# Kernel tuning notes

Measured on AMD Instinct MI355X. Metric: run time of the kernel, lower is better.

The kernel has to match this reference:

```python
import jax, jax.numpy as jnp
import numpy as np

N_NODES, N_EDGES, BATCH, F_IN, GENES = 65536, 262144, 2048, 78, 735
HEADS, HID = 8, 64            # gnn_out_dim = HEADS*HID = 512
GOUT = HEADS * HID
NEG_SLOPE = 0.2
BN_EPS = 1e-5


def setup_inputs() -> dict:
    key = jax.random.key(0)
    ks = jax.random.split(key, 24)
    sc = lambda k, shp, fan: (jax.random.normal(k, shp, jnp.float32) / np.sqrt(fan)).astype(jnp.float32)
    d = {}
    d["x"] = jax.random.normal(ks[0], (N_NODES, F_IN), jnp.float32)
    d["edge_index"] = jax.random.randint(ks[1], (2, N_EDGES), 0, N_NODES)
    d["batch"] = jnp.sort(jax.random.randint(ks[2], (N_NODES,), 0, BATCH))
    d["x_gen"] = jax.random.normal(ks[3], (BATCH, GENES), jnp.float32)
    # GATConv 1: in=78 -> heads*hid
    d["W1"] = sc(ks[4], (F_IN, GOUT), F_IN)
    d["att_src1"] = sc(ks[5], (HEADS, HID), HID)
    d["att_dst1"] = sc(ks[6], (HEADS, HID), HID)
    d["bias1"] = jnp.zeros((GOUT,), jnp.float32)
    # GATConv 2: in=512 -> heads*hid
    d["W2"] = sc(ks[7], (GOUT, GOUT), GOUT)
    d["att_src2"] = sc(ks[8], (HEADS, HID), HID)
    d["att_dst2"] = sc(ks[9], (HEADS, HID), HID)
    d["bias2"] = jnp.zeros((GOUT,), jnp.float32)
    # geno encoder: Linear(735,128) -> BN -> ReLU -> Linear(128,512) -> ReLU
    d["gW1"] = sc(ks[10], (GENES, 2 * HID), GENES)
    d["gb1"] = jnp.zeros((2 * HID,), jnp.float32)
    d["bn_gamma"] = jnp.ones((2 * HID,), jnp.float32)
    d["bn_beta"] = jnp.zeros((2 * HID,), jnp.float32)
    d["bn_mean"] = jnp.zeros((2 * HID,), jnp.float32)
    d["bn_var"] = jnp.ones((2 * HID,), jnp.float32)
    d["gW2"] = sc(ks[11], (2 * HID, GOUT), 2 * HID)
    d["gb2"] = jnp.zeros((GOUT,), jnp.float32)
    # fusion MLP: 1024 -> 256 -> 128 -> 1
    d["fW1"] = sc(ks[12], (2 * GOUT, 256), 2 * GOUT)
    d["fb1"] = jnp.zeros((256,), jnp.float32)
    d["fW2"] = sc(ks[13], (256, 128), 256)
    d["fb2"] = jnp.zeros((128,), jnp.float32)
    d["fW3"] = sc(ks[14], (128, 1), 128)
    d["fb3"] = jnp.zeros((1,), jnp.float32)
    return d


def gat_layer(x, edge_index, W, att_src, att_dst, bias):
    """PyG GATConv (concat=True, add_self_loops=True), eval mode (no dropout)."""
    N = x.shape[0]
    H, C = att_src.shape
    h = (x @ W).reshape(N, H, C)                      # [N,H,C]
    a_src = jnp.einsum('nhc,hc->nh', h, att_src)      # [N,H]
    a_dst = jnp.einsum('nhc,hc->nh', h, att_dst)      # [N,H]
    loop = jnp.arange(N)
    src = jnp.concatenate([edge_index[0], loop])      # [E+N]
    dst = jnp.concatenate([edge_index[1], loop])
    e = jax.nn.leaky_relu(a_src[src] + a_dst[dst], NEG_SLOPE)   # [E+N,H]
    # scatter-softmax over incoming edges per destination node
    e_max = jax.ops.segment_max(e, dst, num_segments=N)
    e = jnp.exp(e - e_max[dst])
    denom = jax.ops.segment_sum(e, dst, num_segments=N)
    alpha = e / (denom[dst] + 1e-16)                  # [E+N,H]
    msg = h[src] * alpha[:, :, None]                  # [E+N,H,C]
    out = jax.ops.segment_sum(msg, dst, num_segments=N)  # [N,H,C]
    return out.reshape(N, H * C) + bias


def global_mean_pool(x, batch, num_graphs):
    sums = jax.ops.segment_sum(x, batch, num_segments=num_graphs)
    cnt = jax.ops.segment_sum(jnp.ones((x.shape[0],), x.dtype), batch, num_segments=num_graphs)
    return sums / jnp.maximum(cnt, 1.0)[:, None]


def reference(x, edge_index, batch, x_gen,
              W1, att_src1, att_dst1, bias1,
              W2, att_src2, att_dst2, bias2,
              gW1, gb1, bn_gamma, bn_beta, bn_mean, bn_var, gW2, gb2,
              fW1, fb1, fW2, fb2, fW3, fb3):
    h = jax.nn.elu(gat_layer(x, edge_index, W1, att_src1, att_dst1, bias1))
    h = jax.nn.elu(gat_layer(h, edge_index, W2, att_src2, att_dst2, bias2))
    g = global_mean_pool(h, batch, BATCH)             # [B, 512]
    # genomic encoder (eval-mode BatchNorm with running stats)
    z = x_gen @ gW1 + gb1
    z = (z - bn_mean) * jax.lax.rsqrt(bn_var + BN_EPS) * bn_gamma + bn_beta
    z = jax.nn.relu(z)
    z = jax.nn.relu(z @ gW2 + gb2)                    # [B, 512]
    c = jnp.concatenate([g, z], axis=1)               # [B, 1024]
    c = jax.nn.relu(c @ fW1 + fb1)
    c = jax.nn.relu(c @ fW2 + fb2)
    return c @ fW3 + fb3                              # [B, 1]
```

## Files before the change

kernel.cpp:

```cpp
#include <hip/hip_runtime.h>
#include <hip/hip_bf16.h>
#include <cstdint>
#include <cstddef>

#define NN 65536
#define NE 262144
#define NB 2048
#define FIN 78
#define GOUTD 512

typedef __bf16 bf16x8 __attribute__((ext_vector_type(8)));
typedef float f32x4 __attribute__((ext_vector_type(4)));

__device__ __forceinline__ float leaky02(float x) { return x > 0.f ? x : 0.2f * x; }
__device__ __forceinline__ void atomAddF(float* p, float v) { unsafeAtomicAdd(p, v); }

__global__ void k_hist(const int* __restrict__ dst, int* __restrict__ deg) {
    int i = blockIdx.x * 256 + threadIdx.x;
    if (i < NE) atomicAdd(&deg[dst[i]], 1);
}

__global__ void k_scan_block(const int* __restrict__ deg, int* __restrict__ ex, int* __restrict__ bsum) {
    __shared__ int s[256];
    int t = threadIdx.x; int g = blockIdx.x * 256 + t;
    int v = deg[g];
    s[t] = v; __syncthreads();
    for (int d = 1; d < 256; d <<= 1) {
        int x = (t >= d) ? s[t - d] : 0;
        __syncthreads();
        s[t] += x;
        __syncthreads();
    }
    ex[g] = s[t] - v;
    if (t == 255) bsum[blockIdx.x] = s[t];
}

__global__ void k_scan_add2(int* __restrict__ rowptr, const int* __restrict__ bsum) {
    __shared__ int s[256];
    int t = threadIdx.x;
    int v = bsum[t];
    s[t] = v; __syncthreads();
    for (int d = 1; d < 256; d <<= 1) {
        int x = (t >= d) ? s[t - d] : 0;
        __syncthreads();
        s[t] += x;
        __syncthreads();
    }
    int prefix = (blockIdx.x == 0) ? 0 : s[blockIdx.x - 1];
    int i = blockIdx.x * 256 + t;
    rowptr[i] += prefix;
    if (i == 0) rowptr[NN] = NE;
}

__global__ void k_scatter(const int* __restrict__ src, const int* __restrict__ dst,
                          const int* __restrict__ rowptr, int* __restrict__ fill,
                          int* __restrict__ colI) {
    int i = blockIdx.x * 256 + threadIdx.x;
    if (i < NE) {
        int d = dst[i];
        int pos = rowptr[d] + atomicAdd(&fill[d], 1);
        colI[pos] = src[i];
    }
}

__global__ void k_cvt_prep(const float* __restrict__ x, const float* __restrict__ W1,
                           const float* __restrict__ W2, __hip_bfloat16* __restrict__ xb,
                           __hip_bfloat16* __restrict__ w1t, __hip_bfloat16* __restrict__ w2t,
                           int* __restrict__ deg, int* __restrict__ fill,
                           const int* __restrict__ batch, int* __restrict__ gstart)
{
    int blk = blockIdx.x;
    if (blk < 16384) {
        int i = blk * 256 + threadIdx.x;
        int row = i >> 6;
        int c = (i & 63) << 1;
        float v0 = (c < FIN) ? x[(size_t)row * FIN + c] : 0.f;
        float v1 = (c + 1 < FIN) ? x[(size_t)row * FIN + c + 1] : 0.f;
        __hip_bfloat16 o[2];
        o[0] = __float2bfloat16(v0);
        o[1] = __float2bfloat16(v1);
        *(uint32_t*)&xb[(size_t)row * 128 + c] = *(const uint32_t*)o;
    } else if (blk < 16640) {
        int i = (blk - 16384) * 256 + threadIdx.x;
        int n = i >> 7, k = i & 127;
        w1t[i] = __float2bfloat16(k < FIN ? W1[(size_t)k * 512 + n] : 0.f);
    } else if (blk < 17664) {
        int i = (blk - 16640) * 256 + threadIdx.x;
        int n = i >> 9, k = i & 511;
        w2t[i] = __float2bfloat16(W2[(size_t)k * 512 + n]);
    } else {
        int i = (blk - 17664) * 256 + threadIdx.x;
        if (i < NN) {
            deg[i] = 0; fill[i] = 0;
            int cur = batch[i];
            int prev = (i == 0) ? -1 : batch[i - 1];
            for (int g = prev + 1; g <= cur; ++g) gstart[g] = i;
            if (i == NN - 1) {
                for (int g = cur + 1; g <= NB; ++g) gstart[g] = NN;
            }
        }
    }
}

__global__ __launch_bounds__(256) void k_mfma_gemm(
    const __hip_bfloat16* __restrict__ A, const __hip_bfloat16* __restrict__ BT,
    __hip_bfloat16* __restrict__ C, int K,
    const float* __restrict__ att_src, const float* __restrict__ att_dst,
    float* __restrict__ a_src, float* __restrict__ a_dst,
    float* __restrict__ t1, float* __restrict__ t2,
    const float* __restrict__ fb1, const float* __restrict__ fb2,
    float* __restrict__ z1)
{
    __shared__ __hip_bfloat16 smem[128 * 128];
    __hip_bfloat16* As = smem;
    __hip_bfloat16* Bs = smem + 128 * 64;
    int tid = threadIdx.x;
    int lane = tid & 63;
    int wave = tid >> 6;
    int id = blockIdx.x;
    int m0 = (((id >> 5) << 3) + (id & 7)) * 128;
    int n0 = ((id >> 3) & 3) * 128;
    int wm = (wave >> 1) * 64;
    int wn = (wave & 1) * 64;
    f32x4 acc[4][4] = {};

    int swz = lane & 7;

    for (int k0 = 0; k0 < K; k0 += 64) {
        #pragma unroll
        for (int c = 0; c < 4; ++c) {
            int off = c * 4096 + tid * 16;
            int r = off >> 7;
            int c16 = (off >> 4) & 7;
            int c16s = c16 ^ (r & 7);
            __builtin_amdgcn_global_load_lds(
                (const __attribute__((address_space(1))) void*)(A + (size_t)(m0 + r) * K + k0 + c16s * 8),
                (__attribute__((address_space(3))) void*)((char*)As + off), 16, 0, 0);
            __builtin_amdgcn_global_load_lds(
                (const __attribute__((address_space(1))) void*)(BT + (size_t)(n0 + r) * K + k0 + c16s * 8),
                (__attribute__((address_space(3))) void*)((char*)Bs + off), 16, 0, 0);
        }
        __syncthreads();
        #pragma unroll
        for (int kk = 0; kk < 64; kk += 32) {
            int c16r = (kk >> 3) + (lane >> 4);
            bf16x8 af[4], bfr[4];
            #pragma unroll
            for (int t = 0; t < 4; ++t) {
                int ra = wm + t * 16 + (lane & 15);
                int rb = wn + t * 16 + (lane & 15);
                af[t]  = *(const bf16x8*)((char*)As + ra * 128 + ((c16r ^ swz) << 4));
                bfr[t] = *(const bf16x8*)((char*)Bs + rb * 128 + ((c16r ^ swz) << 4));
            }
            #pragma unroll
            for (int i = 0; i < 4; ++i)
                #pragma unroll
                for (int j = 0; j < 4; ++j)
                    acc[i][j] = __builtin_amdgcn_mfma_f32_16x16x32_bf16(af[i], bfr[j], acc[i][j], 0, 0, 0);
        }
        __syncthreads();
    }

    int rowb = wm + ((lane >> 4) << 2);
    int colb = wn + (lane & 15);
    #pragma unroll
    for (int i = 0; i < 4; ++i) {
        #pragma unroll
        for (int j = 0; j < 4; ++j) {
            int cc = colb + j * 16;
            #pragma unroll
            for (int r = 0; r < 4; ++r) {
                int rr = rowb + i * 16 + r;
                int word = (cc >> 1) ^ (((rr >> 2) & 7) << 3);
                smem[rr * 128 + word * 2 + (cc & 1)] = __float2bfloat16(acc[i][j][r]);
            }
        }
    }
    __syncthreads();
    #pragma unroll
    for (int cc2 = 0; cc2 < 8; ++cc2) {
        int p = cc2 * 256 + tid;
        int rr = p >> 4;
        int c16 = p & 15;
        int x = ((rr >> 2) & 7) << 3;
        bf16x8 v = *(const bf16x8*)((char*)smem + rr * 256 + ((((c16 << 2) ^ x)) << 2));
        *(bf16x8*)(C + (size_t)(m0 + rr) * 512 + n0 + c16 * 8) = v;
        const float* sp = att_src + n0 + c16 * 8;
        const float* dp = att_dst + n0 + c16 * 8;
        float4 s0 = *(const float4*)sp, s1 = *(const float4*)(sp + 4);
        float4 d0 = *(const float4*)dp, d1 = *(const float4*)(dp + 4);
        float sv[8] = {s0.x, s0.y, s0.z, s0.w, s1.x, s1.y, s1.z, s1.w};
        float dv[8] = {d0.x, d0.y, d0.z, d0.w, d1.x, d1.y, d1.z, d1.w};
        float ps = 0.f, pd = 0.f;
        #pragma unroll
        for (int k = 0; k < 8; ++k) {
            float f = (float)v[k];
            ps = fmaf(f, sv[k], ps);
            pd = fmaf(f, dv[k], pd);
        }
        #pragma unroll
        for (int d = 1; d < 8; d <<= 1) {
            ps += __shfl_xor(ps, d);
            pd += __shfl_xor(pd, d);
        }
        if ((c16 & 7) == 0) {
            int head = (n0 >> 6) + (c16 >> 3);
            a_src[(size_t)(m0 + rr) * 8 + head] = ps;
            a_dst[(size_t)(m0 + rr) * 8 + head] = pd;
        }
    }

    if (t1) {
        if (tid < 64)  *(float4*)(t1 + (size_t)id * 256 + tid * 4) = *(const float4*)(fb1 + tid * 4);
        if (tid < 32)  *(float4*)(t2 + (size_t)id * 128 + tid * 4) = *(const float4*)(fb2 + tid * 4);
        if (tid >= 64 && tid < 96)
            *(float4*)(z1 + (size_t)id * 128 + (tid - 64) * 4) = make_float4(0.f, 0.f, 0.f, 0.f);
    }
}

__global__ __launch_bounds__(256) void k_gat_agg(
    const __hip_bfloat16* __restrict__ h, const float* __restrict__ asrc,
    const float* __restrict__ adst, const int* __restrict__ rowptr,
    const int* __restrict__ colI, const float* __restrict__ bias,
    __hip_bfloat16* __restrict__ out)
{
    int lane = threadIdx.x & 63;
    int n = blockIdx.x * 4 + (threadIdx.x >> 6);
    int start = rowptr[n], end = rowptr[n + 1];
    int hh = lane >> 3;
    float adst_h = adst[n * 8 + hh];
    float acc[8];
    float wsum;
    {
        float w = __expf(leaky02(asrc[n * 8 + hh] + adst_h));
        wsum = w;
        bf16x8 v = *(const bf16x8*)(h + (size_t)n * GOUTD + lane * 8);
        #pragma unroll
        for (int j = 0; j < 8; ++j) acc[j] = w * (float)v[j];
    }
    int i = start;
    for (; i + 1 < end; i += 2) {
        int s0 = colI[i];
        int s1 = colI[i + 1];
        float w0 = __expf(leaky02(asrc[s0 * 8 + hh] + adst_h));
        float w1 = __expf(leaky02(asrc[s1 * 8 + hh] + adst_h));
        bf16x8 v0 = *(const bf16x8*)(h + (size_t)s0 * GOUTD + lane * 8);
        bf16x8 v1 = *(const bf16x8*)(h + (size_t)s1 * GOUTD + lane * 8);
        wsum += w0 + w1;
        #pragma unroll
        for (int j = 0; j < 8; ++j)
            acc[j] = fmaf(w0, (float)v0[j], fmaf(w1, (float)v1[j], acc[j]));
    }
    if (i < end) {
        int s = colI[i];
        float w = __expf(leaky02(asrc[s * 8 + hh] + adst_h));
        wsum += w;
        bf16x8 v = *(const bf16x8*)(h + (size_t)s * GOUTD + lane * 8);
        #pragma unroll
        for (int j = 0; j < 8; ++j) acc[j] = fmaf(w, (float)v[j], acc[j]);
    }
    float rden = 1.f / (wsum + 1e-16f);
    const float* bp = bias + lane * 8;
    float4 b0 = *(const float4*)bp, b1 = *(const float4*)(bp + 4);
    float bb[8] = {b0.x, b0.y, b0.z, b0.w, b1.x, b1.y, b1.z, b1.w};
    __hip_bfloat16 o[8] __attribute__((aligned(16)));
    #pragma unroll
    for (int j = 0; j < 8; ++j) {
        float v = fmaf(acc[j], rden, bb[j]);
        v = (v > 0.f) ? v : (__expf(v) - 1.f);
        o[j] = __float2bfloat16(v);
    }
    *(bf16x8*)(out + (size_t)n * GOUTD + lane * 8) = *(const bf16x8*)o;
}

__global__ __launch_bounds__(512) void k_gat_agg_pool(
    const __hip_bfloat16* __restrict__ h, const float* __restrict__ asrc,
    const float* __restrict__ adst, const int* __restrict__ rowptr,
    const int* __restrict__ colI, const float* __restrict__ bias,
    const int* __restrict__ gstart, float* __restrict__ cfeat)
{
    __shared__ float red[8][512];
    int lane = threadIdx.x & 63;
    int wv = threadIdx.x >> 6;
    int g = blockIdx.x;
    int s = gstart[g], e = gstart[g + 1];
    int hh = lane >> 3;
    const float* bp = bias + lane * 8;
    float4 b0 = *(const float4*)bp, b1 = *(const float4*)(bp + 4);
    float bb[8] = {b0.x, b0.y, b0.z, b0.w, b1.x, b1.y, b1.z, b1.w};
    float psum[8] = {};
    for (int n = s + wv; n < e; n += 8) {
        int start = rowptr[n], end = rowptr[n + 1];
        float adst_h = adst[n * 8 + hh];
        float acc[8];
        float wsum;
        {
            float w = __expf(leaky02(asrc[n * 8 + hh] + adst_h));
            wsum = w;
            bf16x8 v = *(const bf16x8*)(h + (size_t)n * GOUTD + lane * 8);
            #pragma unroll
            for (int j = 0; j < 8; ++j) acc[j] = w * (float)v[j];
        }
        int i = start;
        for (; i + 1 < end; i += 2) {
            int s0 = colI[i];
            int s1 = colI[i + 1];
            float w0 = __expf(leaky02(asrc[s0 * 8 + hh] + adst_h));
            float w1 = __expf(leaky02(asrc[s1 * 8 + hh] + adst_h));
            bf16x8 v0 = *(const bf16x8*)(h + (size_t)s0 * GOUTD + lane * 8);
            bf16x8 v1 = *(const bf16x8*)(h + (size_t)s1 * GOUTD + lane * 8);
            wsum += w0 + w1;
            #pragma unroll
            for (int j = 0; j < 8; ++j)
                acc[j] = fmaf(w0, (float)v0[j], fmaf(w1, (float)v1[j], acc[j]));
        }
        if (i < end) {
            int si = colI[i];
            float w = __expf(leaky02(asrc[si * 8 + hh] + adst_h));
            wsum += w;
            bf16x8 v = *(const bf16x8*)(h + (size_t)si * GOUTD + lane * 8);
            #pragma unroll
            for (int j = 0; j < 8; ++j) acc[j] = fmaf(w, (float)v[j], acc[j]);
        }
        float rden = 1.f / (wsum + 1e-16f);
        #pragma unroll
        for (int j = 0; j < 8; ++j) {
            float v = fmaf(acc[j], rden, bb[j]);
            v = (v > 0.f) ? v : (__expf(v) - 1.f);
            psum[j] += v;
        }
    }
    #pragma unroll
    for (int j = 0; j < 8; ++j) red[wv][lane * 8 + j] = psum[j];
    __syncthreads();
    if (wv == 0) {
        float inv = 1.f / fmaxf((float)(e - s), 1.f);
        float* cp = cfeat + (size_t)g * 1024;
        #pragma unroll
        for (int j = 0; j < 8; ++j) {
            int c = lane * 8 + j;
            float sum = (red[0][c] + red[1][c]) + (red[2][c] + red[3][c])
                      + (red[4][c] + red[5][c]) + (red[6][c] + red[7][c]);
            cp[c] = sum * inv;
        }
    }
}

__global__ __launch_bounds__(256) void k_geno1_sk(
    const float* __restrict__ A, const float* __restrict__ B, float* __restrict__ z1)
{
    __shared__ float As[32][34];
    __shared__ float Bs[32][68];
    int tid = threadIdx.x;
    int n0 = blockIdx.x * 64;
    int m0 = blockIdx.y * 32;
    int kbase = blockIdx.z * 192;
    int am = tid >> 3;
    int ak = (tid & 7) << 2;
    int bk = tid >> 4;
    int bc = (tid & 15) << 2;
    int tm = (tid >> 4) << 1;
    int tn = (tid & 15) << 2;
    float acc[2][4] = {};
    for (int kt = 0; kt < 192; kt += 32) {
        const float* ap = A + (size_t)(m0 + am) * 735 + kbase + kt + ak;
        int kg = kbase + kt + ak;
        As[ak][am]     = (kg     < 735) ? ap[0] : 0.f;
        As[ak + 1][am] = (kg + 1 < 735) ? ap[1] : 0.f;
        As[ak + 2][am] = (kg + 2 < 735) ? ap[2] : 0.f;
        As[ak + 3][am] = (kg + 3 < 735) ? ap[3] : 0.f;
        #pragma unroll
        for (int j = 0; j < 2; ++j) {
            int kr = j * 16 + bk;
            int kgb = kbase + kt + kr;
            float4 b4 = (kgb < 735) ? *(const float4*)(B + (size_t)kgb * 128 + n0 + bc)
                                    : make_float4(0.f, 0.f, 0.f, 0.f);
            *(float4*)&Bs[kr][bc] = b4;
        }
        __syncthreads();
        #pragma unroll
        for (int kk = 0; kk < 32; ++kk) {
            float2 a2 = *(const float2*)&As[kk][tm];
            float4 b4 = *(const float4*)&Bs[kk][tn];
            acc[0][0] = fmaf(a2.x, b4.x, acc[0][0]); acc[0][1] = fmaf(a2.x, b4.y, acc[0][1]);
            acc[0][2] = fmaf(a2.x, b4.z, acc[0][2]); acc[0][3] = fmaf(a2.x, b4.w, acc[0][3]);
            acc[1][0] = fmaf(a2.y, b4.x, acc[1][0]); acc[1][1] = fmaf(a2.y, b4.y, acc[1][1]);
            acc[1][2] = fmaf(a2.y, b4.z, acc[1][2]); acc[1][3] = fmaf(a2.y, b4.w, acc[1][3]);
        }
        __syncthreads();
    }
    #pragma unroll
    for (int i = 0; i < 2; ++i) {
        float* cp = z1 + (size_t)(m0 + tm + i) * 128 + n0 + tn;
        #pragma unroll
        for (int j = 0; j < 4; ++j) atomAddF(cp + j, acc[i][j]);
    }
}

__global__ __launch_bounds__(256) void k_geno2(
    const float* __restrict__ z1, const float* __restrict__ gW2,
    const float* __restrict__ gb1, const float* __restrict__ bn_mean,
    const float* __restrict__ bn_var, const float* __restrict__ bn_gamma,
    const float* __restrict__ bn_beta, const float* __restrict__ gb2,
    float* __restrict__ Cout)
{
    __shared__ float As[32][34];
    __shared__ float Bs[32][68];
    int tid = threadIdx.x;
    int n0 = blockIdx.x * 64;
    int m0 = blockIdx.y * 32;
    int am = tid >> 3;
    int ak = (tid & 7) << 2;
    int bk = tid >> 4;
    int bc = (tid & 15) << 2;
    int tm = (tid >> 4) << 1;
    int tn = (tid & 15) << 2;
    float acc[2][4] = {};
    for (int kt = 0; kt < 128; kt += 32) {
        int kg = kt + ak;
        float4 raw = *(const float4*)(z1 + (size_t)(m0 + am) * 128 + kg);
        float4 g1 = *(const float4*)(gb1 + kg);
        float4 mu = *(const float4*)(bn_mean + kg);
        float4 vr = *(const float4*)(bn_var + kg);
        float4 gm = *(const float4*)(bn_gamma + kg);
        float4 bt = *(const float4*)(bn_beta + kg);
        As[ak][am]     = fmaxf(fmaf(raw.x + g1.x - mu.x, rsqrtf(vr.x + 1e-5f) * gm.x, bt.x), 0.f);
        As[ak + 1][am] = fmaxf(fmaf(raw.y + g1.y - mu.y, rsqrtf(vr.y + 1e-5f) * gm.y, bt.y), 0.f);
        As[ak + 2][am] = fmaxf(fmaf(raw.z + g1.z - mu.z, rsqrtf(vr.z + 1e-5f) * gm.z, bt.z), 0.f);
        As[ak + 3][am] = fmaxf(fmaf(raw.w + g1.w - mu.w, rsqrtf(vr.w + 1e-5f) * gm.w, bt.w), 0.f);
        #pragma unroll
        for (int j = 0; j < 2; ++j) {
            int kr = j * 16 + bk;
            *(float4*)&Bs[kr][bc] = *(const float4*)(gW2 + (size_t)(kt + kr) * 512 + n0 + bc);
        }
        __syncthreads();
        #pragma unroll
        for (int kk = 0; kk < 32; ++kk) {
            float2 a2 = *(const float2*)&As[kk][tm];
            float4 b4 = *(const float4*)&Bs[kk][tn];
            acc[0][0] = fmaf(a2.x, b4.x, acc[0][0]); acc[0][1] = fmaf(a2.x, b4.y, acc[0][1]);
            acc[0][2] = fmaf(a2.x, b4.z, acc[0][2]); acc[0][3] = fmaf(a2.x, b4.w, acc[0][3]);
            acc[1][0] = fmaf(a2.y, b4.x, acc[1][0]); acc[1][1] = fmaf(a2.y, b4.y, acc[1][1]);
            acc[1][2] = fmaf(a2.y, b4.z, acc[1][2]); acc[1][3] = fmaf(a2.y, b4.w, acc[1][3]);
        }
        __syncthreads();
    }
    float4 bb = *(const float4*)(gb2 + n0 + tn);
    #pragma unroll
    for (int i = 0; i < 2; ++i) {
        float* cp = Cout + (size_t)(m0 + tm + i) * 1024 + n0 + tn;
        *(float4*)cp = make_float4(fmaxf(acc[i][0] + bb.x, 0.f), fmaxf(acc[i][1] + bb.y, 0.f),
                                   fmaxf(acc[i][2] + bb.z, 0.f), fmaxf(acc[i][3] + bb.w, 0.f));
    }
}

#define FBM 32
#define FBN 64
#define FKS 32

__global__ __launch_bounds__(256) void k_fgemm_sk(
    const float* __restrict__ A, const float* __restrict__ B,
    float* __restrict__ C, int N, int K, int KS, int reluA)
{
    __shared__ float As[FKS][FBM + 2];
    __shared__ float Bs[FKS][FBN + 4];
    int tid = threadIdx.x;
    int n0 = blockIdx.x * FBN;
    int m0 = blockIdx.y * FBM;
    int kbase = blockIdx.z * KS;
    int am = tid >> 3;
    int ak = (tid & 7) << 2;
    int bk = tid >> 4;
    int bc = (tid & 15) << 2;
    int tm = (tid >> 4) << 1;
    int tn = (tid & 15) << 2;
    float acc[2][4] = {};
    for (int kt = 0; kt < KS; kt += FKS) {
        float4 a4 = *(const float4*)(A + (size_t)(m0 + am) * K + kbase + kt + ak);
        if (reluA) {
            a4.x = fmaxf(a4.x, 0.f); a4.y = fmaxf(a4.y, 0.f);
            a4.z = fmaxf(a4.z, 0.f); a4.w = fmaxf(a4.w, 0.f);
        }
        As[ak][am] = a4.x; As[ak + 1][am] = a4.y;
        As[ak + 2][am] = a4.z; As[ak + 3][am] = a4.w;
        #pragma unroll
        for (int j = 0; j < 2; ++j) {
            int kr = j * 16 + bk;
            *(float4*)&Bs[kr][bc] = *(const float4*)(B + (size_t)(kbase + kt + kr) * N + n0 + bc);
        }
        __syncthreads();
        #pragma unroll
        for (int kk = 0; kk < FKS; ++kk) {
            float2 a2 = *(const float2*)&As[kk][tm];
            float4 b4 = *(const float4*)&Bs[kk][tn];
            acc[0][0] = fmaf(a2.x, b4.x, acc[0][0]); acc[0][1] = fmaf(a2.x, b4.y, acc[0][1]);
            acc[0][2] = fmaf(a2.x, b4.z, acc[0][2]); acc[0][3] = fmaf(a2.x, b4.w, acc[0][3]);
            acc[1][0] = fmaf(a2.y, b4.x, acc[1][0]); acc[1][1] = fmaf(a2.y, b4.y, acc[1][1]);
            acc[1][2] = fmaf(a2.y, b4.z, acc[1][2]); acc[1][3] = fmaf(a2.y, b4.w, acc[1][3]);
        }
        __syncthreads();
    }
    #pragma unroll
    for (int i = 0; i < 2; ++i) {
        float* cp = C + (size_t)(m0 + tm + i) * N + n0 + tn;
        #pragma unroll
        for (int j = 0; j < 4; ++j) atomAddF(cp + j, acc[i][j]);
    }
}

__global__ __launch_bounds__(256) void k_fout(
    const float* __restrict__ t2, const float* __restrict__ fW3,
    const float* __restrict__ fb3, float* __restrict__ out)
{
    int lane = threadIdx.x & 63;
    int row = blockIdx.x * 4 + (threadIdx.x >> 6);
    const float* tp = t2 + (size_t)row * 128;
    float p = fmaxf(tp[lane], 0.f) * fW3[lane] + fmaxf(tp[lane + 64], 0.f) * fW3[lane + 64];
    #pragma unroll
    for (int d = 1; d < 64; d <<= 1) p += __shfl_xor(p, d);
    if (lane == 0) out[row] = p + fb3[0];
}

extern "C" void kernel_launch(void* const* d_in, const int* in_sizes, int n_in,
                              void* d_out, int out_size, void* d_ws, size_t ws_size,
                              hipStream_t stream) {
    const float* x        = (const float*)d_in[0];
    const int*   ei       = (const int*)d_in[1];
    const int*   batch    = (const int*)d_in[2];
    const float* x_gen    = (const float*)d_in[3];
    const float* W1       = (const float*)d_in[4];
    const float* att_src1 = (const float*)d_in[5];
    const float* att_dst1 = (const float*)d_in[6];
    const float* bias1    = (const float*)d_in[7];
    const float* W2       = (const float*)d_in[8];
    const float* att_src2 = (const float*)d_in[9];
    const float* att_dst2 = (const float*)d_in[10];
    const float* bias2    = (const float*)d_in[11];
    const float* gW1      = (const float*)d_in[12];
    const float* gb1      = (const float*)d_in[13];
    const float* bn_gamma = (const float*)d_in[14];
    const float* bn_beta  = (const float*)d_in[15];
    const float* bn_mean  = (const float*)d_in[16];
    const float* bn_var   = (const float*)d_in[17];
    const float* gW2      = (const float*)d_in[18];
    const float* gb2      = (const float*)d_in[19];
    const float* fW1      = (const float*)d_in[20];
    const float* fb1      = (const float*)d_in[21];
    const float* fW2      = (const float*)d_in[22];
    const float* fb2      = (const float*)d_in[23];
    const float* fW3      = (const float*)d_in[24];
    const float* fb3      = (const float*)d_in[25];
    float* out = (float*)d_out;

    const int* srcv = ei;
    const int* dstv = ei + NE;

    char* w = (char*)d_ws;
    size_t off = 0;
    auto take = [&](size_t bytes) -> void* {
        void* p = w + off;
        off += (bytes + 255) & ~(size_t)255;
        return p;
    };
    __hip_bfloat16* hbuf = (__hip_bfloat16*)take((size_t)NN * GOUTD * 2);
    __hip_bfloat16* abuf = (__hip_bfloat16*)take((size_t)NN * GOUTD * 2);
    __hip_bfloat16* xb   = (__hip_bfloat16*)take((size_t)NN * 128 * 2);
    __hip_bfloat16* w1t  = (__hip_bfloat16*)take((size_t)512 * 128 * 2);
    __hip_bfloat16* w2t  = (__hip_bfloat16*)take((size_t)512 * 512 * 2);
    float* asrc   = (float*)take((size_t)NN * 8 * 4);
    float* adst   = (float*)take((size_t)NN * 8 * 4);
    int*   rowptr = (int*)take((size_t)(NN + 1) * 4);
    int*   colI   = (int*)take((size_t)NE * 4);
    int*   deg    = (int*)take((size_t)NN * 4);
    int*   fill   = (int*)take((size_t)NN * 4);
    int*   bsum   = (int*)take(256 * 4);
    int*   gstart = (int*)take((NB + 1) * 4);
    float* cbuf = (float*)xb;
    float* z1   = cbuf + (size_t)2048 * 1024;
    float* t1   = z1 + (size_t)2048 * 128;
    float* t2   = t1 + (size_t)2048 * 256;

    k_cvt_prep<<<17920, 256, 0, stream>>>(x, W1, W2, xb, w1t, w2t, deg, fill, batch, gstart);
    k_hist<<<NE / 256, 256, 0, stream>>>(dstv, deg);
    k_scan_block<<<256, 256, 0, stream>>>(deg, rowptr, bsum);
    k_scan_add2<<<256, 256, 0, stream>>>(rowptr, bsum);
    k_scatter<<<NE / 256, 256, 0, stream>>>(srcv, dstv, rowptr, fill, colI);

    k_mfma_gemm<<<2048, 256, 0, stream>>>(xb, w1t, hbuf, 128, att_src1, att_dst1, asrc, adst,
                                          nullptr, nullptr, nullptr, nullptr, nullptr);
    k_gat_agg<<<NN / 4, 256, 0, stream>>>(hbuf, asrc, adst, rowptr, colI, bias1, abuf);

    k_mfma_gemm<<<2048, 256, 0, stream>>>(abuf, w2t, hbuf, 512, att_src2, att_dst2, asrc, adst,
                                          t1, t2, fb1, fb2, z1);

    k_gat_agg_pool<<<NB, 512, 0, stream>>>(hbuf, asrc, adst, rowptr, colI, bias2,
                                           gstart, cbuf);

    k_geno1_sk<<<dim3(2, 64, 4), 256, 0, stream>>>(x_gen, gW1, z1);
    k_geno2<<<dim3(8, 64), 256, 0, stream>>>(z1, gW2, gb1, bn_mean, bn_var, bn_gamma,
                                             bn_beta, gb2, cbuf + 512);

    k_fgemm_sk<<<dim3(4, 64, 4), 256, 0, stream>>>(cbuf, fW1, t1, 256, 1024, 256, 0);
    k_fgemm_sk<<<dim3(2, 64, 4), 256, 0, stream>>>(t1, fW2, t2, 128, 256, 64, 1);
    k_fout<<<NB / 4, 256, 0, stream>>>(t2, fW3, fb3, out);
}
```

Baseline: 443.9 us.

## Widen GEMM tile to 128x256 with 8 waves and shrink pool blocks

```diff
diff --git a/kernel.cpp b/kernel.cpp
--- a/kernel.cpp
+++ b/kernel.cpp
@@ -102,7 +102,7 @@
     }
 }
 
-__global__ __launch_bounds__(256) void k_mfma_gemm(
+__global__ __launch_bounds__(512) void k_mfma_gemm(
     const __hip_bfloat16* __restrict__ A, const __hip_bfloat16* __restrict__ BT,
     __hip_bfloat16* __restrict__ C, int K,
     const float* __restrict__ att_src, const float* __restrict__ att_dst,
@@ -111,31 +111,40 @@
     const float* __restrict__ fb1, const float* __restrict__ fb2,
     float* __restrict__ z1)
 {
-    __shared__ __hip_bfloat16 smem[128 * 128];
+    __shared__ __hip_bfloat16 smem[128 * 64 + 256 * 64];
     __hip_bfloat16* As = smem;
     __hip_bfloat16* Bs = smem + 128 * 64;
     int tid = threadIdx.x;
     int lane = tid & 63;
     int wave = tid >> 6;
+    int wr = wave >> 2;
+    int wc = wave & 3;
     int id = blockIdx.x;
-    int m0 = (((id >> 5) << 3) + (id & 7)) * 128;
-    int n0 = ((id >> 3) & 3) * 128;
-    int wm = (wave >> 1) * 64;
-    int wn = (wave & 1) * 64;
+    int m0 = (((id >> 4) << 3) + (id & 7)) * 128;
+    int n0 = ((id >> 3) & 1) * 256;
+    int wm = wr * 64;
+    int wn = wc * 64;
     f32x4 acc[4][4] = {};
 
     int swz = lane & 7;
 
     for (int k0 = 0; k0 < K; k0 += 64) {
         #pragma unroll
-        for (int c = 0; c < 4; ++c) {
-            int off = c * 4096 + tid * 16;
+        for (int c = 0; c < 2; ++c) {
+            int off = c * 8192 + tid * 16;
             int r = off >> 7;
             int c16 = (off >> 4) & 7;
             int c16s = c16 ^ (r & 7);
             __builtin_amdgcn_global_load_lds(
                 (const __attribute__((address_space(1))) void*)(A + (size_t)(m0 + r) * K + k0 + c16s * 8),
                 (__attribute__((address_space(3))) void*)((char*)As + off), 16, 0, 0);
+        }
+        #pragma unroll
+        for (int c = 0; c < 4; ++c) {
+            int off = c * 8192 + tid * 16;
+            int r = off >> 7;
+            int c16 = (off >> 4) & 7;
+            int c16s = c16 ^ (r & 7);
             __builtin_amdgcn_global_load_lds(
                 (const __attribute__((address_space(1))) void*)(BT + (size_t)(n0 + r) * K + k0 + c16s * 8),
                 (__attribute__((address_space(3))) void*)((char*)Bs + off), 16, 0, 0);
@@ -161,60 +170,73 @@
         __syncthreads();
     }
 
-    int rowb = wm + ((lane >> 4) << 2);
-    int colb = wn + (lane & 15);
     #pragma unroll
-    for (int i = 0; i < 4; ++i) {
-        #pragma unroll
-        for (int j = 0; j < 4; ++j) {
-            int cc = colb + j * 16;
-            #pragma unroll
-            for (int r = 0; r < 4; ++r) {
-                int rr = rowb + i * 16 + r;
-                int word = (cc >> 1) ^ (((rr >> 2) & 7) << 3);
-                smem[rr * 128 + word * 2 + (cc & 1)] = __float2bfloat16(acc[i][j][r]);
+    for (int p = 0; p < 2; ++p) {
+        if ((wc >> 1) == p) {
+            int rowb = wm + ((lane >> 4) << 2);
+            int colb = (wc & 1) * 64 + (lane & 15);
+            #pragma unroll
+            for (int i = 0; i < 4; ++i) {
+                #pragma unroll
+                for (int j = 0; j < 4; ++j) {
+                    int cc = colb + j * 16;
+                    #pragma unroll
+                    for (int r = 0; r < 4; ++r) {
+                        int rr = rowb + i * 16 + r;
+                        int word = (cc >> 1) ^ (((rr >> 2) & 7) << 3);
+                        smem[rr * 128 + word * 2 + (cc & 1)] = __float2bfloat16(acc[i][j][r]);
+                    }
+                }
             }
         }
-    }
-    __syncthreads();
-    #pragma unroll
-    for (int cc2 = 0; cc2 < 8; ++cc2) {
-        int p = cc2 * 256 + tid;
-        int rr = p >> 4;
-        int c16 = p & 15;
-        int x = ((rr >> 2) & 7) << 3;
-        bf16x8 v = *(const bf16x8*)((char*)smem + rr * 256 + ((((c16 << 2) ^ x)) << 2));
-        *(bf16x8*)(C + (size_t)(m0 + rr) * 512 + n0 + c16 * 8) = v;
-        const float* sp = att_src + n0 + c16 * 8;
-        const float* dp = att_dst + n0 + c16 * 8;
-        float4 s0 = *(const float4*)sp, s1 = *(const float4*)(sp + 4);
-        float4 d0 = *(const float4*)dp, d1 = *(const float4*)(dp + 4);
-        float sv[8] = {s0.x, s0.y, s0.z, s0.w, s1.x, s1.y, s1.z, s1.w};
-        float dv[8] = {d0.x, d0.y, d0.z, d0.w, d1.x, d1.y, d1.z, d1.w};
-        float ps = 0.f, pd = 0.f;
-        #pragma unroll
-        for (int k = 0; k < 8; ++k) {
-            float f = (float)v[k];
-            ps = fmaf(f, sv[k], ps);
-            pd = fmaf(f, dv[k], pd);
-        }
-        #pragma unroll
-        for (int d = 1; d < 8; d <<= 1) {
-            ps += __shfl_xor(ps, d);
-            pd += __shfl_xor(pd, d);
-        }
-        if ((c16 & 7) == 0) {
-            int head = (n0 >> 6) + (c16 >> 3);
-            a_src[(size_t)(m0 + rr) * 8 + head] = ps;
-            a_dst[(size_t)(m0 + rr) * 8 + head] = pd;
-        }
+        __syncthreads();
+        int cb = n0 + p * 128;
+        #pragma unroll
+        for (int cc2 = 0; cc2 < 4; ++cc2) {
+            int pi = cc2 * 512 + tid;
+            int rr = pi >> 4;
+            int c16 = pi & 15;
+            int x = ((rr >> 2) & 7) << 3;
+            bf16x8 v = *(const bf16x8*)((char*)smem + rr * 256 + ((((c16 << 2) ^ x)) << 2));
+            *(bf16x8*)(C + (size_t)(m0 + rr) * 512 + cb + c16 * 8) = v;
+            const float* sp = att_src + cb + c16 * 8;
+            const float* dp = att_dst + cb + c16 * 8;
+            float4 s0 = *(const float4*)sp, s1 = *(const float4*)(sp + 4);
+            float4 d0 = *(const float4*)dp, d1 = *(const float4*)(dp + 4);
+            float sv[8] = {s0.x, s0.y, s0.z, s0.w, s1.x, s1.y, s1.z, s1.w};
+            float dv[8] = {d0.x, d0.y, d0.z, d0.w, d1.x, d1.y, d1.z, d1.w};
+            float ps = 0.f, pd = 0.f;
+            #pragma unroll
+            for (int k = 0; k < 8; ++k) {
+                float f = (float)v[k];
+                ps = fmaf(f, sv[k], ps);
+                pd = fmaf(f, dv[k], pd);
+            }
+            #pragma unroll
+            for (int d = 1; d < 8; d <<= 1) {
+                ps += __shfl_xor(ps, d);
+                pd += __shfl_xor(pd, d);
+            }
+            if ((c16 & 7) == 0) {
+                int head = (cb >> 6) + (c16 >> 3);
+                a_src[(size_t)(m0 + rr) * 8 + head] = ps;
+                a_dst[(size_t)(m0 + rr) * 8 + head] = pd;
+            }
+        }
+        __syncthreads();
     }
 
     if (t1) {
-        if (tid < 64)  *(float4*)(t1 + (size_t)id * 256 + tid * 4) = *(const float4*)(fb1 + tid * 4);
-        if (tid < 32)  *(float4*)(t2 + (size_t)id * 128 + tid * 4) = *(const float4*)(fb2 + tid * 4);
-        if (tid >= 64 && tid < 96)
-            *(float4*)(z1 + (size_t)id * 128 + (tid - 64) * 4) = make_float4(0.f, 0.f, 0.f, 0.f);
+        if (tid < 128) {
+            int r = 2 * id + (tid >> 6), e = tid & 63;
+            *(float4*)(t1 + (size_t)r * 256 + e * 4) = *(const float4*)(fb1 + e * 4);
+        } else if (tid < 192) {
+            int q = tid - 128, r = 2 * id + (q >> 5), e = q & 31;
+            *(float4*)(t2 + (size_t)r * 128 + e * 4) = *(const float4*)(fb2 + e * 4);
+        } else if (tid < 256) {
+            int q = tid - 192, r = 2 * id + (q >> 5), e = q & 31;
+            *(float4*)(z1 + (size_t)r * 128 + e * 4) = make_float4(0.f, 0.f, 0.f, 0.f);
+        }
     }
 }
 
@@ -273,13 +295,13 @@
     *(bf16x8*)(out + (size_t)n * GOUTD + lane * 8) = *(const bf16x8*)o;
 }
 
-__global__ __launch_bounds__(512) void k_gat_agg_pool(
+__global__ __launch_bounds__(256) void k_gat_agg_pool(
     const __hip_bfloat16* __restrict__ h, const float* __restrict__ asrc,
     const float* __restrict__ adst, const int* __restrict__ rowptr,
     const int* __restrict__ colI, const float* __restrict__ bias,
     const int* __restrict__ gstart, float* __restrict__ cfeat)
 {
-    __shared__ float red[8][512];
+    __shared__ float red[4][512];
     int lane = threadIdx.x & 63;
     int wv = threadIdx.x >> 6;
     int g = blockIdx.x;
@@ -289,7 +311,7 @@
     float4 b0 = *(const float4*)bp, b1 = *(const float4*)(bp + 4);
     float bb[8] = {b0.x, b0.y, b0.z, b0.w, b1.x, b1.y, b1.z, b1.w};
     float psum[8] = {};
-    for (int n = s + wv; n < e; n += 8) {
+    for (int n = s + wv; n < e; n += 4) {
         int start = rowptr[n], end = rowptr[n + 1];
         float adst_h = adst[n * 8 + hh];
         float acc[8];
@@ -339,9 +361,7 @@
         #pragma unroll
         for (int j = 0; j < 8; ++j) {
             int c = lane * 8 + j;
-            float sum = (red[0][c] + red[1][c]) + (red[2][c] + red[3][c])
-                      + (red[4][c] + red[5][c]) + (red[6][c] + red[7][c]);
-            cp[c] = sum * inv;
+            cp[c] = (red[0][c] + red[1][c] + red[2][c] + red[3][c]) * inv;
         }
     }
 }
@@ -586,14 +606,14 @@
     k_scan_add2<<<256, 256, 0, stream>>>(rowptr, bsum);
     k_scatter<<<NE / 256, 256, 0, stream>>>(srcv, dstv, rowptr, fill, colI);
 
-    k_mfma_gemm<<<2048, 256, 0, stream>>>(xb, w1t, hbuf, 128, att_src1, att_dst1, asrc, adst,
+    k_mfma_gemm<<<1024, 512, 0, stream>>>(xb, w1t, hbuf, 128, att_src1, att_dst1, asrc, adst,
                                           nullptr, nullptr, nullptr, nullptr, nullptr);
     k_gat_agg<<<NN / 4, 256, 0, stream>>>(hbuf, asrc, adst, rowptr, colI, bias1, abuf);
 
-    k_mfma_gemm<<<2048, 256, 0, stream>>>(abuf, w2t, hbuf, 512, att_src2, att_dst2, asrc, adst,
+    k_mfma_gemm<<<1024, 512, 0, stream>>>(abuf, w2t, hbuf, 512, att_src2, att_dst2, asrc, adst,
                                           t1, t2, fb1, fb2, z1);
 
-    k_gat_agg_pool<<<NB, 512, 0, stream>>>(hbuf, asrc, adst, rowptr, colI, bias2,
+    k_gat_agg_pool<<<NB, 256, 0, stream>>>(hbuf, asrc, adst, rowptr, colI, bias2,
                                            gstart, cbuf);
 
     k_geno1_sk<<<dim3(2, 64, 4), 256, 0, stream>>>(x_gen, gW1, z1);
```

Result: no change. 438.6 us (-1.2%).
